# Kernel optimization log

Measured on AMD Instinct MI355X. Metric: run time of the kernel, lower is better.

The kernel has to match this reference:

```python
import jax, jax.numpy as jnp
import numpy as np

N_NODES = 100000
N_EDGES = 1600000
N_GRAPHS = 256
IN_F = 64   # global_features (GNN input dim)
OUT_F = 64  # node_features (GNN output dim)


def setup_inputs() -> dict:
    key = jax.random.key(0)
    ks = jax.random.split(key, 8)
    x = jax.random.normal(ks[0], (N_NODES, IN_F), dtype=jnp.float32)
    edge_index = jax.random.randint(ks[1], (2, N_EDGES), 0, N_NODES, dtype=jnp.int64)
    batch = jnp.sort(jax.random.randint(ks[2], (N_NODES,), 0, N_GRAPHS, dtype=jnp.int64))
    # GNNLayer linear: in=global_features, out=node_features
    W_gnn = jax.random.normal(ks[3], (IN_F, OUT_F), dtype=jnp.float32) / np.sqrt(IN_F)
    b_gnn = jnp.zeros((OUT_F,), dtype=jnp.float32)
    # global_attention: Linear(node_features, 1)
    W_att = jax.random.normal(ks[4], (OUT_F, 1), dtype=jnp.float32) / np.sqrt(OUT_F)
    b_att = jnp.zeros((1,), dtype=jnp.float32)
    return {"x": x, "edge_index": edge_index, "batch": batch,
            "W_gnn": W_gnn, "b_gnn": b_gnn, "W_att": W_att, "b_att": b_att}


def reference(x, edge_index, batch, W_gnn, b_gnn, W_att, b_att):
    src, dst = edge_index[0], edge_index[1]
    # --- GNN message passing layer: aggregate neighbor features, transform ---
    agg = jax.ops.segment_sum(x[src], dst, num_segments=N_NODES)  # [N, IN_F]
    h = jax.nn.relu((x + agg) @ W_gnn + b_gnn)                    # [N, OUT_F]
    # --- attention scores + scatter softmax over batch segments ---
    scores = (h @ W_att + b_att)[:, 0]                            # [N]
    seg_max = jax.ops.segment_max(scores, batch, num_segments=N_GRAPHS)
    e = jnp.exp(scores - seg_max[batch])
    denom = jax.ops.segment_sum(e, batch, num_segments=N_GRAPHS)
    w = e / denom[batch]                                          # [N]
    # --- weighted scatter-add pooling ---
    out = jax.ops.segment_sum(w[:, None] * h, batch, num_segments=N_GRAPHS)
    return out  # [N_GRAPHS, OUT_F]
```

## Files before the change

### kernel.cpp

```cpp
#include <hip/hip_runtime.h>

#define N_NODES  100000
#define N_EDGES  1600000
#define N_GRAPHS 256
#define F        64

#define BSHIFT   8
#define BNODES   256
#define NBUCKET  391
#define CHUNK    8192
#define NCHUNK   196

__device__ __forceinline__ unsigned short f2bf(float f) {
    unsigned int u = __float_as_uint(f);
    u += 0x7FFFu + ((u >> 16) & 1u);
    return (unsigned short)(u >> 16);
}
__global__ __launch_bounds__(256) void cast_kernel(
        const float* __restrict__ x, unsigned short* __restrict__ xh) {
    int i = blockIdx.x * 256 + threadIdx.x;
    float4 v = ((const float4*)x)[i];
    ushort4 o;
    o.x = f2bf(v.x); o.y = f2bf(v.y); o.z = f2bf(v.z); o.w = f2bf(v.w);
    ((ushort4*)xh)[i] = o;
}

__global__ __launch_bounds__(1024) void hist_kernel(
        const int* __restrict__ dst, int* __restrict__ cnt) {
    __shared__ int hist[NBUCKET];
    int tid = threadIdx.x;
    for (int b = tid; b < NBUCKET; b += 1024) hist[b] = 0;
    __syncthreads();
    int base = blockIdx.x * CHUNK;
    int end  = min(base + CHUNK, N_EDGES);
    for (int e = base + tid; e < end; e += 1024)
        atomicAdd(&hist[dst[e] >> BSHIFT], 1);
    __syncthreads();
    for (int b = tid; b < NBUCKET; b += 1024)
        cnt[blockIdx.x * NBUCKET + b] = hist[b];
}

__global__ __launch_bounds__(512) void chunk_scan_kernel(
        const int* __restrict__ cnt, int* __restrict__ start, int* __restrict__ bbase) {
    __shared__ int t[512];
    int b = threadIdx.x;
    int tot = 0;
    if (b < NBUCKET)
        for (int c = 0; c < NCHUNK; ++c) tot += cnt[c * NBUCKET + b];
    t[b] = (b < NBUCKET) ? tot : 0;
    __syncthreads();
    #pragma unroll
    for (int o = 1; o < 512; o <<= 1) {
        int u = (b >= o) ? t[b - o] : 0;
        __syncthreads();
        t[b] += u;
        __syncthreads();
    }
    if (b < NBUCKET) {
        int base = t[b] - tot;
        bbase[b] = base;
        if (b == NBUCKET - 1) bbase[NBUCKET] = t[b];
        int run = base;
        for (int c = 0; c < NCHUNK; ++c) {
            start[c * NBUCKET + b] = run;
            run += cnt[c * NBUCKET + b];
        }
    }
}

__global__ __launch_bounds__(1024) void scatter_kernel(
        const int* __restrict__ src, const int* __restrict__ dst,
        const int* __restrict__ start, unsigned int* __restrict__ pairs) {
    __shared__ int cur[NBUCKET];
    int tid = threadIdx.x;
    for (int b = tid; b < NBUCKET; b += 1024)
        cur[b] = start[blockIdx.x * NBUCKET + b];
    __syncthreads();
    int base = blockIdx.x * CHUNK;
    int end  = min(base + CHUNK, N_EDGES);
    for (int e = base + tid; e < end; e += 1024) {
        int d = dst[e];
        int slot = atomicAdd(&cur[d >> BSHIFT], 1);
        pairs[slot] = ((unsigned)(d & (BNODES - 1)) << 17) | (unsigned)src[e];
    }
}

__global__ __launch_bounds__(1024) void bucket_sort_kernel(
        const unsigned int* __restrict__ pairs,
        const int* __restrict__ bbase,
        int* __restrict__ eidx, int* __restrict__ noff) {
    __shared__ int cnt[BNODES];
    __shared__ int pref[BNODES];
    __shared__ int cur[BNODES];
    int tid = threadIdx.x;
    int b = blockIdx.x;
    int lo = bbase[b], hi = bbase[b + 1];

    if (tid < BNODES) cnt[tid] = 0;
    __syncthreads();
    for (int e = lo + tid; e < hi; e += 1024)
        atomicAdd(&cnt[pairs[e] >> 17], 1);
    __syncthreads();
    if (tid < BNODES) pref[tid] = cnt[tid];
    __syncthreads();
    #pragma unroll
    for (int o = 1; o < BNODES; o <<= 1) {
        int u = (tid < BNODES && tid >= o) ? pref[tid - o] : 0;
        __syncthreads();
        if (tid < BNODES) pref[tid] += u;
        __syncthreads();
    }
    if (tid < BNODES) {
        int excl = lo + pref[tid] - cnt[tid];
        cur[tid] = excl;
        int node = b * BNODES + tid;
        if (node < N_NODES) noff[node] = excl;
        if (node == N_NODES - 1) noff[N_NODES] = hi;
    }
    __syncthreads();
    for (int e = lo + tid; e < hi; e += 1024) {
        unsigned int p = pairs[e];
        int slot = atomicAdd(&cur[p >> 17], 1);
        eidx[slot] = (int)(p & 0x1FFFFu);
    }
}

#define NODES_PER_WAVE 25
#define GT_NWAVES  (N_NODES / NODES_PER_WAVE)
#define GT_BLOCKS  (GT_NWAVES / 4)

__device__ __forceinline__ float bfl(unsigned int u) {
    return __uint_as_float(u << 16);
}
__device__ __forceinline__ float bfh(unsigned int u) {
    return __uint_as_float(u & 0xFFFF0000u);
}

__global__ __launch_bounds__(256) void gather_pool_kernel(
        const unsigned short* __restrict__ xh,
        const int*   __restrict__ noff,
        const int*   __restrict__ eidx,
        const int*   __restrict__ batch,
        const float* __restrict__ Wg,
        const float* __restrict__ bg,
        const float* __restrict__ Wa,
        const float* __restrict__ ba,
        float*       __restrict__ out_acc,
        float*       __restrict__ denom) {
    int tid  = threadIdx.x;
    int lane = tid & 63;
    int grp  = lane >> 3;
    int c    = lane & 7;
    int waveId = blockIdx.x * 4 + (tid >> 6);

    int n0 = waveId * NODES_PER_WAVE;
    if (n0 >= N_NODES) return;
    int nEnd = n0 + NODES_PER_WAVE;

    float wcol[F];
    #pragma unroll
    for (int k = 0; k < F; ++k) wcol[k] = Wg[k * F + lane];
    float bgl = bg[lane];
    float wal = Wa[lane];
    float ba0 = ba[0];

    const uint4* xh4 = (const uint4*)xh;

    int   cur_g = batch[n0];
    float accw  = 0.f;
    float denw  = 0.f;

    for (int n = n0; n < nEnd; ++n) {
        int start = noff[n];
        int end   = noff[n + 1];

        float a0=0.f,a1=0.f,a2=0.f,a3=0.f,a4=0.f,a5=0.f,a6=0.f,a7=0.f;
        for (int base = start; base < end; base += 64) {
            int jmax = end - base; if (jmax > 64) jmax = 64;
            int sl = (base + lane < end) ? eidx[base + lane] : 0;
            for (int j = 0; j < jmax; j += 8) {
                int el = j + grp;
                int s  = __shfl(sl, el, 64);
                if (el < jmax) {
                    uint4 v = xh4[s * 8 + c];
                    a0 += bfl(v.x); a1 += bfh(v.x);
                    a2 += bfl(v.y); a3 += bfh(v.y);
                    a4 += bfl(v.z); a5 += bfh(v.z);
                    a6 += bfl(v.w); a7 += bfh(v.w);
                }
            }
        }
        #pragma unroll
        for (int o = 8; o <= 32; o <<= 1) {
            a0 += __shfl_xor(a0, o, 64); a1 += __shfl_xor(a1, o, 64);
            a2 += __shfl_xor(a2, o, 64); a3 += __shfl_xor(a3, o, 64);
            a4 += __shfl_xor(a4, o, 64); a5 += __shfl_xor(a5, o, 64);
            a6 += __shfl_xor(a6, o, 64); a7 += __shfl_xor(a7, o, 64);
        }
        {
            uint4 v = xh4[n * 8 + c];
            a0 += bfl(v.x); a1 += bfh(v.x);
            a2 += bfl(v.y); a3 += bfh(v.y);
            a4 += bfl(v.z); a5 += bfh(v.z);
            a6 += bfl(v.w); a7 += bfh(v.w);
        }

        float re[8] = {a0,a1,a2,a3,a4,a5,a6,a7};
        float q0=0.f,q1=0.f,q2=0.f,q3=0.f,q4=0.f,q5=0.f,q6=0.f,q7=0.f;
        #pragma unroll
        for (int k = 0; k < F; k += 8) {
            int ln = k >> 3;
            q0 += __int_as_float(__builtin_amdgcn_readlane(__float_as_int(re[0]), ln)) * wcol[k + 0];
            q1 += __int_as_float(__builtin_amdgcn_readlane(__float_as_int(re[1]), ln)) * wcol[k + 1];
            q2 += __int_as_float(__builtin_amdgcn_readlane(__float_as_int(re[2]), ln)) * wcol[k + 2];
            q3 += __int_as_float(__builtin_amdgcn_readlane(__float_as_int(re[3]), ln)) * wcol[k + 3];
            q4 += __int_as_float(__builtin_amdgcn_readlane(__float_as_int(re[4]), ln)) * wcol[k + 4];
            q5 += __int_as_float(__builtin_amdgcn_readlane(__float_as_int(re[5]), ln)) * wcol[k + 5];
            q6 += __int_as_float(__builtin_amdgcn_readlane(__float_as_int(re[6]), ln)) * wcol[k + 6];
            q7 += __int_as_float(__builtin_amdgcn_readlane(__float_as_int(re[7]), ln)) * wcol[k + 7];
        }
        float hv = ((q0 + q1) + (q2 + q3)) + ((q4 + q5) + (q6 + q7)) + bgl;
        hv = hv > 0.f ? hv : 0.f;

        float p = hv * wal;
        #pragma unroll
        for (int o = 32; o > 0; o >>= 1)
            p += __shfl_down(p, o, 64);
        float s = __int_as_float(__builtin_amdgcn_readlane(__float_as_int(p), 0)) + ba0;
        float e = __expf(s);

        int g = batch[n];
        if (g != cur_g) {
            atomicAdd(&out_acc[cur_g * F + lane], accw);
            if (lane == 0) atomicAdd(&denom[cur_g], denw);
            accw = 0.f; denw = 0.f; cur_g = g;
        }
        accw += e * hv;
        denw += e;
    }
    atomicAdd(&out_acc[cur_g * F + lane], accw);
    if (lane == 0) atomicAdd(&denom[cur_g], denw);
}

__global__ __launch_bounds__(256) void finalize_kernel(
        float* __restrict__ out, const float* __restrict__ denom) {
    int i = blockIdx.x * 256 + threadIdx.x;
    if (i >= N_GRAPHS * F) return;
    float d = denom[i >> 6];
    out[i] = (d > 0.f) ? out[i] / d : 0.f;
}

extern "C" void kernel_launch(void* const* d_in, const int* in_sizes, int n_in,
                              void* d_out, int out_size, void* d_ws, size_t ws_size,
                              hipStream_t stream) {
    const float* x     = (const float*)d_in[0];
    const int*   ei    = (const int*)d_in[1];
    const int*   batch = (const int*)d_in[2];
    const float* Wg    = (const float*)d_in[3];
    const float* bg    = (const float*)d_in[4];
    const float* Wa    = (const float*)d_in[5];
    const float* ba    = (const float*)d_in[6];
    float* out = (float*)d_out;

    const int* src = ei;
    const int* dst = ei + N_EDGES;

    char* ws = (char*)d_ws;
    int*            cnt    = (int*)(ws);
    int*            start  = (int*)(ws +   306688);
    int*            bbase  = (int*)(ws +   613376);
    unsigned int*   pairs  = (unsigned int*)(ws +  615168);
    int*            eidx   = (int*)(ws +  7015168);
    int*            noff   = (int*)(ws + 13415168);
    float*          denom  = (float*)(ws + 13815424);
    unsigned short* xh     = (unsigned short*)(ws + 13816448);

    hipMemsetAsync(out,   0, (size_t)N_GRAPHS * F * sizeof(float), stream);
    hipMemsetAsync(denom, 0, N_GRAPHS * sizeof(float), stream);

    cast_kernel        <<<(N_NODES * F / 4) / 256, 256, 0, stream>>>(x, xh);
    hist_kernel        <<<NCHUNK, 1024, 0, stream>>>(dst, cnt);
    chunk_scan_kernel  <<<1, 512, 0, stream>>>(cnt, start, bbase);
    scatter_kernel     <<<NCHUNK, 1024, 0, stream>>>(src, dst, start, pairs);
    bucket_sort_kernel <<<NBUCKET, 1024, 0, stream>>>(pairs, bbase, eidx, noff);
    gather_pool_kernel <<<GT_BLOCKS, 256, 0, stream>>>(
        xh, noff, eidx, batch, Wg, bg, Wa, ba, out, denom);
    finalize_kernel    <<<(N_GRAPHS * F + 255) / 256, 256, 0, stream>>>(out, denom);
}
```

Baseline: 218.0 us.

## Fuse CSR build into per-chunk local sort and in-block bucket gather

Replaces the four-kernel global counting sort (histogram, chunk scan, scatter, bucket sort) with one per-chunk kernel. That kernel sorts each chunk's edges by 128-node bucket in shared memory and writes them back contiguously, along with a transposed table of chunk/bucket start offsets. The gather kernel then has each block collect its bucket's segments from all 196 chunks into LDS and counting-sort them by node locally before the gather/GEMV/pooling. This removes two launches, the global scatter with poor write locality, and the global eidx/noff round trip. It relies on a fixed EDGE_CAP of 2560 edges per 128-node bucket, which could overflow for skewed inputs, and uses large LDS per block, which may limit occupancy.

```diff
diff --git a/kernel.cpp b/kernel.cpp
--- a/kernel.cpp
+++ b/kernel.cpp
@@ -5,11 +5,11 @@
 #define N_GRAPHS 256
 #define F        64
 
-#define BSHIFT   8
-#define BNODES   256
-#define NBUCKET  391
 #define CHUNK    8192
 #define NCHUNK   196
+#define GBN      128
+#define NB2      782
+#define EDGE_CAP 2560
 
 __device__ __forceinline__ unsigned short f2bf(float f) {
     unsigned int u = __float_as_uint(f);
@@ -25,121 +25,56 @@
     ((ushort4*)xh)[i] = o;
 }
 
-__global__ __launch_bounds__(1024) void hist_kernel(
-        const int* __restrict__ dst, int* __restrict__ cnt) {
-    __shared__ int hist[NBUCKET];
-    int tid = threadIdx.x;
-    for (int b = tid; b < NBUCKET; b += 1024) hist[b] = 0;
-    __syncthreads();
-    int base = blockIdx.x * CHUNK;
-    int end  = min(base + CHUNK, N_EDGES);
-    for (int e = base + tid; e < end; e += 1024)
-        atomicAdd(&hist[dst[e] >> BSHIFT], 1);
-    __syncthreads();
-    for (int b = tid; b < NBUCKET; b += 1024)
-        cnt[blockIdx.x * NBUCKET + b] = hist[b];
-}
-
-__global__ __launch_bounds__(512) void chunk_scan_kernel(
-        const int* __restrict__ cnt, int* __restrict__ start, int* __restrict__ bbase) {
-    __shared__ int t[512];
-    int b = threadIdx.x;
-    int tot = 0;
-    if (b < NBUCKET)
-        for (int c = 0; c < NCHUNK; ++c) tot += cnt[c * NBUCKET + b];
-    t[b] = (b < NBUCKET) ? tot : 0;
-    __syncthreads();
-    #pragma unroll
-    for (int o = 1; o < 512; o <<= 1) {
-        int u = (b >= o) ? t[b - o] : 0;
-        __syncthreads();
-        t[b] += u;
-        __syncthreads();
-    }
-    if (b < NBUCKET) {
-        int base = t[b] - tot;
-        bbase[b] = base;
-        if (b == NBUCKET - 1) bbase[NBUCKET] = t[b];
-        int run = base;
-        for (int c = 0; c < NCHUNK; ++c) {
-            start[c * NBUCKET + b] = run;
-            run += cnt[c * NBUCKET + b];
-        }
-    }
-}
-
-__global__ __launch_bounds__(1024) void scatter_kernel(
+__global__ __launch_bounds__(1024) void scatter_sort_kernel(
         const int* __restrict__ src, const int* __restrict__ dst,
-        const int* __restrict__ start, unsigned int* __restrict__ pairs) {
-    __shared__ int cur[NBUCKET];
-    int tid = threadIdx.x;
-    for (int b = tid; b < NBUCKET; b += 1024)
-        cur[b] = start[blockIdx.x * NBUCKET + b];
-    __syncthreads();
-    int base = blockIdx.x * CHUNK;
-    int end  = min(base + CHUNK, N_EDGES);
-    for (int e = base + tid; e < end; e += 1024) {
-        int d = dst[e];
-        int slot = atomicAdd(&cur[d >> BSHIFT], 1);
-        pairs[slot] = ((unsigned)(d & (BNODES - 1)) << 17) | (unsigned)src[e];
-    }
-}
-
-__global__ __launch_bounds__(1024) void bucket_sort_kernel(
-        const unsigned int* __restrict__ pairs,
-        const int* __restrict__ bbase,
-        int* __restrict__ eidx, int* __restrict__ noff) {
-    __shared__ int cnt[BNODES];
-    __shared__ int pref[BNODES];
-    __shared__ int cur[BNODES];
-    int tid = threadIdx.x;
-    int b = blockIdx.x;
-    int lo = bbase[b], hi = bbase[b + 1];
-
-    if (tid < BNODES) cnt[tid] = 0;
-    __syncthreads();
-    for (int e = lo + tid; e < hi; e += 1024)
-        atomicAdd(&cnt[pairs[e] >> 17], 1);
-    __syncthreads();
-    if (tid < BNODES) pref[tid] = cnt[tid];
-    __syncthreads();
-    #pragma unroll
-    for (int o = 1; o < BNODES; o <<= 1) {
-        int u = (tid < BNODES && tid >= o) ? pref[tid - o] : 0;
-        __syncthreads();
-        if (tid < BNODES) pref[tid] += u;
-        __syncthreads();
-    }
-    if (tid < BNODES) {
-        int excl = lo + pref[tid] - cnt[tid];
+        unsigned int* __restrict__ pairs, int* __restrict__ cstartT) {
+    __shared__ int hist[NB2];
+    __shared__ int cur[NB2];
+    __shared__ int scan[1024];
+    __shared__ unsigned int stage[CHUNK];
+    int tid  = threadIdx.x;
+    int c    = blockIdx.x;
+    int base = c * CHUNK;
+    int m    = min(CHUNK, N_EDGES - base);
+
+    for (int b = tid; b < NB2; b += 1024) hist[b] = 0;
+    __syncthreads();
+    for (int e = tid; e < m; e += 1024)
+        atomicAdd(&hist[dst[base + e] >> 7], 1);
+    __syncthreads();
+    scan[tid] = (tid < NB2) ? hist[tid] : 0;
+    __syncthreads();
+    #pragma unroll
+    for (int o = 1; o < 1024; o <<= 1) {
+        int u = (tid >= o) ? scan[tid - o] : 0;
+        __syncthreads();
+        scan[tid] += u;
+        __syncthreads();
+    }
+    if (tid < NB2) {
+        int excl = scan[tid] - hist[tid];
         cur[tid] = excl;
-        int node = b * BNODES + tid;
-        if (node < N_NODES) noff[node] = excl;
-        if (node == N_NODES - 1) noff[N_NODES] = hi;
-    }
-    __syncthreads();
-    for (int e = lo + tid; e < hi; e += 1024) {
-        unsigned int p = pairs[e];
-        int slot = atomicAdd(&cur[p >> 17], 1);
-        eidx[slot] = (int)(p & 0x1FFFFu);
-    }
-}
-
-#define NODES_PER_WAVE 25
-#define GT_NWAVES  (N_NODES / NODES_PER_WAVE)
-#define GT_BLOCKS  (GT_NWAVES / 4)
-
-__device__ __forceinline__ float bfl(unsigned int u) {
-    return __uint_as_float(u << 16);
-}
-__device__ __forceinline__ float bfh(unsigned int u) {
-    return __uint_as_float(u & 0xFFFF0000u);
-}
-
-__global__ __launch_bounds__(256) void gather_pool_kernel(
+        cstartT[tid * NCHUNK + c] = base + excl;
+    }
+    if (tid == 0) cstartT[NB2 * NCHUNK + c] = base + m;
+    __syncthreads();
+    for (int e = tid; e < m; e += 1024) {
+        int d = dst[base + e];
+        int slot = atomicAdd(&cur[d >> 7], 1);
+        stage[slot] = ((unsigned)(d & (GBN - 1)) << 17) | (unsigned)src[base + e];
+    }
+    __syncthreads();
+    for (int e = tid; e < m; e += 1024)
+        pairs[base + e] = stage[e];
+}
+
+__device__ __forceinline__ float bfl(unsigned int u) { return __uint_as_float(u << 16); }
+__device__ __forceinline__ float bfh(unsigned int u) { return __uint_as_float(u & 0xFFFF0000u); }
+
+__global__ __launch_bounds__(512) void gather_pool_kernel(
         const unsigned short* __restrict__ xh,
-        const int*   __restrict__ noff,
-        const int*   __restrict__ eidx,
+        const unsigned int*   __restrict__ pairs,
+        const int*   __restrict__ cstartT,
         const int*   __restrict__ batch,
         const float* __restrict__ Wg,
         const float* __restrict__ bg,
@@ -147,15 +82,81 @@
         const float* __restrict__ ba,
         float*       __restrict__ out_acc,
         float*       __restrict__ denom) {
-    int tid  = threadIdx.x;
-    int lane = tid & 63;
-    int grp  = lane >> 3;
-    int c    = lane & 7;
-    int waveId = blockIdx.x * 4 + (tid >> 6);
-
-    int n0 = waveId * NODES_PER_WAVE;
-    if (n0 >= N_NODES) return;
-    int nEnd = n0 + NODES_PER_WAVE;
+    __shared__ int rstart[NCHUNK];
+    __shared__ int rcnt[NCHUNK];
+    __shared__ int roff[NCHUNK];
+    __shared__ int sc[256];
+    __shared__ int Etot_s;
+    __shared__ unsigned int epairs[EDGE_CAP];
+    __shared__ unsigned int esrc[EDGE_CAP];
+    __shared__ int ncnt[GBN];
+    __shared__ int nstart[GBN];
+    __shared__ int ncur[GBN];
+
+    int tid   = threadIdx.x;
+    int wave  = tid >> 6;
+    int lane  = tid & 63;
+    int b     = blockIdx.x;
+    int node0 = b * GBN;
+    int nn    = min(GBN, N_NODES - node0);
+
+    if (tid < NCHUNK) {
+        int a = cstartT[b * NCHUNK + tid];
+        int n = cstartT[(b + 1) * NCHUNK + tid];
+        rstart[tid] = a;
+        rcnt[tid]   = n - a;
+    }
+    __syncthreads();
+    if (tid < 256) sc[tid] = (tid < NCHUNK) ? rcnt[tid] : 0;
+    __syncthreads();
+    #pragma unroll
+    for (int o = 1; o < 256; o <<= 1) {
+        int u = (tid < 256 && tid >= o) ? sc[tid - o] : 0;
+        __syncthreads();
+        if (tid < 256) sc[tid] += u;
+        __syncthreads();
+    }
+    if (tid < NCHUNK) roff[tid] = sc[tid] - rcnt[tid];
+    if (tid == 0) Etot_s = sc[NCHUNK - 1];
+    __syncthreads();
+    int E = Etot_s;
+
+    for (int r = wave; r < NCHUNK; r += 8) {
+        int cr = rcnt[r];
+        for (int l = lane; l < cr; l += 64)
+            epairs[roff[r] + l] = pairs[rstart[r] + l];
+    }
+    __syncthreads();
+
+    if (tid < GBN) ncnt[tid] = 0;
+    __syncthreads();
+    for (int e = tid; e < E; e += 512)
+        atomicAdd(&ncnt[epairs[e] >> 17], 1);
+    __syncthreads();
+    if (tid < 128) sc[tid] = ncnt[tid];
+    __syncthreads();
+    #pragma unroll
+    for (int o = 1; o < 128; o <<= 1) {
+        int u = (tid < 128 && tid >= o) ? sc[tid - o] : 0;
+        __syncthreads();
+        if (tid < 128) sc[tid] += u;
+        __syncthreads();
+    }
+    if (tid < GBN) {
+        int excl = sc[tid] - ncnt[tid];
+        nstart[tid] = excl;
+        ncur[tid]   = excl;
+    }
+    __syncthreads();
+    for (int e = tid; e < E; e += 512) {
+        unsigned int p = epairs[e];
+        int slot = atomicAdd(&ncur[p >> 17], 1);
+        esrc[slot] = p & 0x1FFFFu;
+    }
+    __syncthreads();
+
+    int grp = lane >> 3;
+    int cc  = lane & 7;
 
     float wcol[F];
     #pragma unroll
@@ -166,80 +167,85 @@
 
     const uint4* xh4 = (const uint4*)xh;
 
-    int   cur_g = batch[n0];
-    float accw  = 0.f;
-    float denw  = 0.f;
-
-    for (int n = n0; n < nEnd; ++n) {
-        int start = noff[n];
-        int end   = noff[n + 1];
-
-        float a0=0.f,a1=0.f,a2=0.f,a3=0.f,a4=0.f,a5=0.f,a6=0.f,a7=0.f;
-        for (int base = start; base < end; base += 64) {
-            int jmax = end - base; if (jmax > 64) jmax = 64;
-            int sl = (base + lane < end) ? eidx[base + lane] : 0;
-            for (int j = 0; j < jmax; j += 8) {
-                int el = j + grp;
-                int s  = __shfl(sl, el, 64);
-                if (el < jmax) {
-                    uint4 v = xh4[s * 8 + c];
-                    a0 += bfl(v.x); a1 += bfh(v.x);
-                    a2 += bfl(v.y); a3 += bfh(v.y);
-                    a4 += bfl(v.z); a5 += bfh(v.z);
-                    a6 += bfl(v.w); a7 += bfh(v.w);
+    int r0 = wave * 16;
+    if (r0 < nn) {
+        int rEnd = min(r0 + 16, nn);
+        int   cur_g = batch[node0 + r0];
+        float accw  = 0.f;
+        float denw  = 0.f;
+
+        for (int r = r0; r < rEnd; ++r) {
+            int n     = node0 + r;
+            int start = nstart[r];
+            int end   = start + ncnt[r];
+
+            float a0=0.f,a1=0.f,a2=0.f,a3=0.f,a4=0.f,a5=0.f,a6=0.f,a7=0.f;
+            for (int bs = start; bs < end; bs += 64) {
+                int jmax = end - bs; if (jmax > 64) jmax = 64;
+                int sl = (bs + lane < end) ? (int)esrc[bs + lane] : 0;
+                for (int j = 0; j < jmax; j += 8) {
+                    int el = j + grp;
+                    int s  = __shfl(sl, el, 64);
+                    if (el < jmax) {
+                        uint4 v = xh4[s * 8 + cc];
+                        a0 += bfl(v.x); a1 += bfh(v.x);
+                        a2 += bfl(v.y); a3 += bfh(v.y);
+                        a4 += bfl(v.z); a5 += bfh(v.z);
+                        a6 += bfl(v.w); a7 += bfh(v.w);
+                    }
                 }
             }
+            #pragma unroll
+            for (int o = 8; o <= 32; o <<= 1) {
+                a0 += __shfl_xor(a0, o, 64); a1 += __shfl_xor(a1, o, 64);
+                a2 += __shfl_xor(a2, o, 64); a3 += __shfl_xor(a3, o, 64);
+                a4 += __shfl_xor(a4, o, 64); a5 += __shfl_xor(a5, o, 64);
+                a6 += __shfl_xor(a6, o, 64); a7 += __shfl_xor(a7, o, 64);
+            }
+            {
+                uint4 v = xh4[n * 8 + cc];
+                a0 += bfl(v.x); a1 += bfh(v.x);
+                a2 += bfl(v.y); a3 += bfh(v.y);
+                a4 += bfl(v.z); a5 += bfh(v.z);
+                a6 += bfl(v.w); a7 += bfh(v.w);
+            }
+
+            float re[8] = {a0,a1,a2,a3,a4,a5,a6,a7};
+            float q0=0.f,q1=0.f,q2=0.f,q3=0.f,q4=0.f,q5=0.f,q6=0.f,q7=0.f;
+            #pragma unroll
+            for (int k = 0; k < F; k += 8) {
+                int ln = k >> 3;
+                q0 += __int_as_float(__builtin_amdgcn_readlane(__float_as_int(re[0]), ln)) * wcol[k + 0];
+                q1 += __int_as_float(__builtin_amdgcn_readlane(__float_as_int(re[1]), ln)) * wcol[k + 1];
+                q2 += __int_as_float(__builtin_amdgcn_readlane(__float_as_int(re[2]), ln)) * wcol[k + 2];
+                q3 += __int_as_float(__builtin_amdgcn_readlane(__float_as_int(re[3]), ln)) * wcol[k + 3];
+                q4 += __int_as_float(__builtin_amdgcn_readlane(__float_as_int(re[4]), ln)) * wcol[k + 4];
+                q5 += __int_as_float(__builtin_amdgcn_readlane(__float_as_int(re[5]), ln)) * wcol[k + 5];
+                q6 += __int_as_float(__builtin_amdgcn_readlane(__float_as_int(re[6]), ln)) * wcol[k + 6];
+                q7 += __int_as_float(__builtin_amdgcn_readlane(__float_as_int(re[7]), ln)) * wcol[k + 7];
+            }
+            float hv = ((q0 + q1) + (q2 + q3)) + ((q4 + q5) + (q6 + q7)) + bgl;
+            hv = hv > 0.f ? hv : 0.f;
+
+            float p = hv * wal;
+            #pragma unroll
+            for (int o = 32; o > 0; o >>= 1)
+                p += __shfl_down(p, o, 64);
+            float s = __int_as_float(__builtin_amdgcn_readlane(__float_as_int(p), 0)) + ba0;
+            float e = __expf(s);
+
+            int g = batch[n];
+            if (g != cur_g) {
+                atomicAdd(&out_acc[cur_g * F + lane], accw);
+                if (lane == 0) atomicAdd(&denom[cur_g], denw);
+                accw = 0.f; denw = 0.f; cur_g = g;
+            }
+            accw += e * hv;
+            denw += e;
         }
-        #pragma unroll
-        for (int o = 8; o <= 32; o <<= 1) {
-            a0 += __shfl_xor(a0, o, 64); a1 += __shfl_xor(a1, o, 64);
-            a2 += __shfl_xor(a2, o, 64); a3 += __shfl_xor(a3, o, 64);
-            a4 += __shfl_xor(a4, o, 64); a5 += __shfl_xor(a5, o, 64);
-            a6 += __shfl_xor(a6, o, 64); a7 += __shfl_xor(a7, o, 64);
-        }
-        {
-            uint4 v = xh4[n * 8 + c];
-            a0 += bfl(v.x); a1 += bfh(v.x);
-            a2 += bfl(v.y); a3 += bfh(v.y);
-            a4 += bfl(v.z); a5 += bfh(v.z);
-            a6 += bfl(v.w); a7 += bfh(v.w);
-        }
-
-        float re[8] = {a0,a1,a2,a3,a4,a5,a6,a7};
-        float q0=0.f,q1=0.f,q2=0.f,q3=0.f,q4=0.f,q5=0.f,q6=0.f,q7=0.f;
-        #pragma unroll
-        for (int k = 0; k < F; k += 8) {
-            int ln = k >> 3;
-            q0 += __int_as_float(__builtin_amdgcn_readlane(__float_as_int(re[0]), ln)) * wcol[k + 0];
-            q1 += __int_as_float(__builtin_amdgcn_readlane(__float_as_int(re[1]), ln)) * wcol[k + 1];
-            q2 += __int_as_float(__builtin_amdgcn_readlane(__float_as_int(re[2]), ln)) * wcol[k + 2];
-            q3 += __int_as_float(__builtin_amdgcn_readlane(__float_as_int(re[3]), ln)) * wcol[k + 3];
-            q4 += __int_as_float(__builtin_amdgcn_readlane(__float_as_int(re[4]), ln)) * wcol[k + 4];
-            q5 += __int_as_float(__builtin_amdgcn_readlane(__float_as_int(re[5]), ln)) * wcol[k + 5];
-            q6 += __int_as_float(__builtin_amdgcn_readlane(__float_as_int(re[6]), ln)) * wcol[k + 6];
-            q7 += __int_as_float(__builtin_amdgcn_readlane(__float_as_int(re[7]), ln)) * wcol[k + 7];
-        }
-        float hv = ((q0 + q1) + (q2 + q3)) + ((q4 + q5) + (q6 + q7)) + bgl;
-        hv = hv > 0.f ? hv : 0.f;
-
-        float p = hv * wal;
-        #pragma unroll
-        for (int o = 32; o > 0; o >>= 1)
-            p += __shfl_down(p, o, 64);
-        float s = __int_as_float(__builtin_amdgcn_readlane(__float_as_int(p), 0)) + ba0;
-        float e = __expf(s);
-
-        int g = batch[n];
-        if (g != cur_g) {
-            atomicAdd(&out_acc[cur_g * F + lane], accw);
-            if (lane == 0) atomicAdd(&denom[cur_g], denw);
-            accw = 0.f; denw = 0.f; cur_g = g;
-        }
-        accw += e * hv;
-        denw += e;
-    }
-    atomicAdd(&out_acc[cur_g * F + lane], accw);
-    if (lane == 0) atomicAdd(&denom[cur_g], denw);
+        atomicAdd(&out_acc[cur_g * F + lane], accw);
+        if (lane == 0) atomicAdd(&denom[cur_g], denw);
+    }
 }
 
 __global__ __launch_bounds__(256) void finalize_kernel(
@@ -266,24 +272,17 @@
     const int* dst = ei + N_EDGES;
 
     char* ws = (char*)d_ws;
-    int*            cnt    = (int*)(ws);
-    int*            start  = (int*)(ws +   306688);
-    int*            bbase  = (int*)(ws +   613376);
-    unsigned int*   pairs  = (unsigned int*)(ws +  615168);
-    int*            eidx   = (int*)(ws +  7015168);
-    int*            noff   = (int*)(ws + 13415168);
-    float*          denom  = (float*)(ws + 13815424);
-    unsigned short* xh     = (unsigned short*)(ws + 13816448);
+    unsigned short* xh      = (unsigned short*)(ws);
+    unsigned int*   pairs   = (unsigned int*)(ws + 12800000);
+    int*            cstartT = (int*)(ws + 19200000);
+    float*          denom   = (float*)(ws + 19814144);
 
     hipMemsetAsync(out,   0, (size_t)N_GRAPHS * F * sizeof(float), stream);
     hipMemsetAsync(denom, 0, N_GRAPHS * sizeof(float), stream);
 
     cast_kernel        <<<(N_NODES * F / 4) / 256, 256, 0, stream>>>(x, xh);
-    hist_kernel        <<<NCHUNK, 1024, 0, stream>>>(dst, cnt);
-    chunk_scan_kernel  <<<1, 512, 0, stream>>>(cnt, start, bbase);
-    scatter_kernel     <<<NCHUNK, 1024, 0, stream>>>(src, dst, start, pairs);
-    bucket_sort_kernel <<<NBUCKET, 1024, 0, stream>>>(pairs, bbase, eidx, noff);
-    gather_pool_kernel <<<GT_BLOCKS, 256, 0, stream>>>(
-        xh, noff, eidx, batch, Wg, bg, Wa, ba, out, denom);
+    scatter_sort_kernel<<<NCHUNK, 1024, 0, stream>>>(src, dst, pairs, cstartT);
+    gather_pool_kernel <<<NB2, 512, 0, stream>>>(
+        xh, pairs, cstartT, batch, Wg, bg, Wa, ba, out, denom);
     finalize_kernel    <<<(N_GRAPHS * F + 255) / 256, 256, 0, stream>>>(out, denom);
 }
```

Result: no change. 218.4 us (+0.2%).
